# Kernel optimization log

Measured on AMD Instinct MI355X. Metric: run time of the kernel, lower is better.

## Reference

```python
import jax, jax.numpy as jnp
import numpy as np

N, Wt, Tt, DIM = 16, 256, 2048, 256
EPS = 1e-5

def silu(x):
    return x * jax.nn.sigmoid(x)

def setup_inputs() -> dict:
    key = jax.random.key(0)
    ks = jax.random.split(key, 12)
    d = {}
    d['T'] = jnp.arange(Tt, dtype=jnp.float32)
    d['durations'] = jax.random.uniform(ks[0], (N, Wt, 1), jnp.float32)
    d['features'] = jax.random.normal(ks[1], (N, Wt, DIM), jnp.float32)
    d['conv1_w'] = jax.random.normal(ks[2], (8, DIM, 3), jnp.float32) * 0.05
    d['conv1_b'] = jnp.zeros((8,), jnp.float32)
    d['bn1_g'] = jnp.ones((8,), jnp.float32)
    d['bn1_b'] = jnp.zeros((8,), jnp.float32)
    d['bn1_m'] = jnp.zeros((8,), jnp.float32)
    d['bn1_v'] = jnp.ones((8,), jnp.float32)
    d['conv2_w'] = jax.random.normal(ks[3], (8, DIM, 3), jnp.float32) * 0.05
    d['conv2_b'] = jnp.zeros((8,), jnp.float32)
    d['bn2_g'] = jnp.ones((8,), jnp.float32)
    d['bn2_b'] = jnp.zeros((8,), jnp.float32)
    d['bn2_m'] = jnp.zeros((8,), jnp.float32)
    d['bn2_v'] = jnp.ones((8,), jnp.float32)
    d['sb1_w1'] = jax.random.normal(ks[4], (10, 2), jnp.float32) * 0.3
    d['sb1_b1'] = jnp.zeros((2,), jnp.float32)
    d['sb1_w2'] = jax.random.normal(ks[5], (2, 2), jnp.float32) * 0.3
    d['sb1_b2'] = jnp.zeros((2,), jnp.float32)
    d['sb2_w1'] = jax.random.normal(ks[6], (10, 16), jnp.float32) * 0.3
    d['sb2_b1'] = jnp.zeros((16,), jnp.float32)
    d['sb2_w2'] = jax.random.normal(ks[7], (16, 16), jnp.float32) * 0.3
    d['sb2_b2'] = jnp.zeros((16,), jnp.float32)
    d['proj1_w'] = jax.random.normal(ks[8], (2, DIM), jnp.float32) * 0.3
    d['proj1_b'] = jnp.zeros((DIM,), jnp.float32)
    d['proj2_w'] = jax.random.normal(ks[9], (16, 1), jnp.float32) * 0.3
    d['proj2_b'] = jnp.zeros((1,), jnp.float32)
    return d

def _conv_bn_silu(x_ncw, w, b, g, beta, m, v):
    # Conv1d(dim->8, k=3, pad=1) + BatchNorm(eval) + SiLU
    y = jax.lax.conv_general_dilated(x_ncw, w, (1,), [(1, 1)],
                                     dimension_numbers=('NCH', 'OIH', 'NCH'))
    y = y + b[None, :, None]
    y = (y - m[None, :, None]) * jax.lax.rsqrt(v[None, :, None] + EPS)
    y = y * g[None, :, None] + beta[None, :, None]
    return silu(y)

def _swish_block(x, w1, b1, w2, b2):
    x = silu(x @ w1 + b1)
    return silu(x @ w2 + b2)

def reference(T, durations, features, conv1_w, conv1_b, bn1_g, bn1_b, bn1_m, bn1_v,
              conv2_w, conv2_b, bn2_g, bn2_b, bn2_m, bn2_v,
              sb1_w1, sb1_b1, sb1_w2, sb1_b2, sb2_w1, sb2_b1, sb2_w2, sb2_b2,
              proj1_w, proj1_b, proj2_w, proj2_b):
    feat = jnp.swapaxes(features, 1, 2)  # (N, C, W)
    n, _, w = feat.shape
    t = T.shape[0]
    left = jnp.swapaxes(_conv_bn_silu(feat, conv1_w, conv1_b, bn1_g, bn1_b, bn1_m, bn1_v), 1, 2)   # (N, W, 8)
    right = jnp.swapaxes(_conv_bn_silu(feat, conv2_w, conv2_b, bn2_g, bn2_b, bn2_m, bn2_v), 1, 2)  # (N, W, 8)
    token_end = jnp.cumsum(durations, axis=1)        # (N, W, 1)
    token_start = token_end - durations              # (N, W, 1)
    S = T[None, None, :] - token_start               # (N, W, T)
    E = token_end - T[None, None, :]                 # (N, W, T)
    left_b = jnp.broadcast_to(left[:, :, None, :], (n, w, t, 8))
    right_b = jnp.broadcast_to(right[:, :, None, :], (n, w, t, 8))
    xleft = jnp.concatenate([S[..., None], E[..., None], left_b], axis=-1)    # (N, W, T, 10)
    xright = jnp.concatenate([S[..., None], E[..., None], right_b], axis=-1)  # (N, W, T, 10)
    C = _swish_block(xleft, sb1_w1, sb1_b1, sb1_w2, sb1_b2)                   # (N, W, T, 2)
    xr = _swish_block(xright, sb2_w1, sb2_b1, sb2_w2, sb2_b2)                 # (N, W, T, 16)
    score = (xr @ proj2_w + proj2_b)[..., 0]                                  # (N, W, T)
    Wsm = jax.nn.softmax(score, axis=1)  # softmax over tokens W
    out_r = jnp.einsum('nkt,ndk->ntd', Wsm, feat)                             # (N, T, dim)
    out_l = jnp.einsum('nkt,nktp->ntp', Wsm, C) @ proj1_w + proj1_b           # (N, T, dim)
    return out_l + out_r
```

## Files before the change

kernel.cpp:

```cpp
#include <hip/hip_runtime.h>
#include <hip/hip_bf16.h>

#define NN  16
#define WT  256
#define TT  2048
#define DIM 256
#define TBT 8

typedef __attribute__((ext_vector_type(8))) short short8_t;
typedef __attribute__((ext_vector_type(4))) float f32x4;

__device__ __forceinline__ float fast_rcp(float x){ return __builtin_amdgcn_rcpf(x); }

__device__ __forceinline__ float silu_f(float x){
    return x * fast_rcp(1.0f + __expf(-x));
}

__device__ __forceinline__ unsigned short f2bf(float x){
    union { float f; unsigned u; } v; v.f = x;
    unsigned r = v.u + 0x7FFFu + ((v.u >> 16) & 1u);
    return (unsigned short)(r >> 16);
}

__device__ __forceinline__ void fma4(float4& a, float s, const float4& f){
    a.x = fmaf(s, f.x, a.x); a.y = fmaf(s, f.y, a.y);
    a.z = fmaf(s, f.z, a.z); a.w = fmaf(s, f.w, a.w);
}

__global__ __launch_bounds__(WT) void cumsum_k(const float* __restrict__ dur,
                                               float* __restrict__ ts,
                                               float* __restrict__ te){
    int n = blockIdx.x, w = threadIdx.x;
    __shared__ float s[WT];
    float d = dur[n*WT + w];
    s[w] = d;
    __syncthreads();
    for (int off = 1; off < WT; off <<= 1){
        float v = (w >= off) ? s[w-off] : 0.0f;
        __syncthreads();
        s[w] += v;
        __syncthreads();
    }
    float e = s[w];
    te[n*WT + w] = e;
    ts[n*WT + w] = e - d;
}

__global__ __launch_bounds__(256) void prep_k(
    const float* __restrict__ feat,
    const float* __restrict__ c1w, const float* __restrict__ c1b,
    const float* __restrict__ g1,  const float* __restrict__ be1,
    const float* __restrict__ m1,  const float* __restrict__ vv1,
    const float* __restrict__ c2w, const float* __restrict__ c2b,
    const float* __restrict__ g2,  const float* __restrict__ be2,
    const float* __restrict__ m2,  const float* __restrict__ vv2,
    const float* __restrict__ sb1w1, const float* __restrict__ sb1b1,
    const float* __restrict__ sb2w1, const float* __restrict__ sb2b1,
    const float* __restrict__ ts, const float* __restrict__ te,
    float* __restrict__ v1o, float* __restrict__ v2o)
{
    int w = blockIdx.x, n = blockIdx.y;
    int tid = threadIdx.x;
    const float* fb = feat + (size_t)(n*WT)*DIM;
    float fm = (w > 0)    ? fb[(size_t)(w-1)*DIM + tid] : 0.0f;
    float f0 =              fb[(size_t) w   *DIM + tid];
    float fp = (w < WT-1) ? fb[(size_t)(w+1)*DIM + tid] : 0.0f;

    float pl[8], pr[8];
    #pragma unroll
    for (int o = 0; o < 8; o++){
        const float* wp = c1w + (size_t)(o*DIM + tid)*3;
        pl[o] = fmaf(fm, wp[0], fmaf(f0, wp[1], fp*wp[2]));
        const float* wq = c2w + (size_t)(o*DIM + tid)*3;
        pr[o] = fmaf(fm, wq[0], fmaf(f0, wq[1], fp*wq[2]));
    }
    #pragma unroll
    for (int o = 0; o < 8; o++){
        #pragma unroll
        for (int off = 32; off; off >>= 1){
            pl[o] += __shfl_xor(pl[o], off);
            pr[o] += __shfl_xor(pr[o], off);
        }
    }
    __shared__ float sws[4][16];
    int wave = tid >> 6, lane = tid & 63;
    if (lane == 0){
        #pragma unroll
        for (int o = 0; o < 8; o++){ sws[wave][o] = pl[o]; sws[wave][8+o] = pr[o]; }
    }
    __syncthreads();
    __shared__ float slr[16];
    if (tid < 16){
        float s = sws[0][tid] + sws[1][tid] + sws[2][tid] + sws[3][tid];
        int o = tid & 7; bool isr = tid >= 8;
        float bias = isr ? c2b[o] : c1b[o];
        float mm   = isr ? m2[o]  : m1[o];
        float vv   = isr ? vv2[o] : vv1[o];
        float gg   = isr ? g2[o]  : g1[o];
        float bb   = isr ? be2[o] : be1[o];
        float y = s + bias;
        y = (y - mm) * rsqrtf(vv + 1e-5f);
        y = y * gg + bb;
        slr[tid] = silu_f(y);
    }
    __syncthreads();
    float start = ts[n*WT + w], end = te[n*WT + w];
    if (tid < 16){
        int j = tid;
        float acc = sb2b1[j] - start*sb2w1[j] + end*sb2w1[16 + j];
        #pragma unroll
        for (int o = 0; o < 8; o++) acc = fmaf(slr[8+o], sb2w1[(2+o)*16 + j], acc);
        v2o[(size_t)(n*WT + w)*16 + j] = acc;
    } else if (tid < 18){
        int p = tid - 16;
        float acc = sb1b1[p] - start*sb1w1[p] + end*sb1w1[2 + p];
        #pragma unroll
        for (int o = 0; o < 8; o++) acc = fmaf(slr[o], sb1w1[(2+o)*2 + p], acc);
        v1o[(size_t)(n*WT + w)*2 + p] = acc;
    }
}

__global__ __launch_bounds__(256) void featpack_k(const float* __restrict__ feat,
                                                  unsigned short* __restrict__ featP)
{
    int kb = blockIdx.x, n = blockIdx.y;
    int d = threadIdx.x;
    const float* fb = feat + (size_t)n*WT*DIM + (size_t)kb*32*DIM + d;
    unsigned short* op = featP + ((size_t)(n*8 + kb)*DIM + d)*32;
    unsigned short buf[32];
    #pragma unroll
    for (int e = 0; e < 32; e++) buf[e] = f2bf(fb[(size_t)e*DIM]);
    #pragma unroll
    for (int g = 0; g < 4; g++){
        uint4 u;
        u.x = (unsigned)buf[g*8+0] | ((unsigned)buf[g*8+1] << 16);
        u.y = (unsigned)buf[g*8+2] | ((unsigned)buf[g*8+3] << 16);
        u.z = (unsigned)buf[g*8+4] | ((unsigned)buf[g*8+5] << 16);
        u.w = (unsigned)buf[g*8+6] | ((unsigned)buf[g*8+7] << 16);
        *(uint4*)(op + g*8) = u;
    }
}

__global__ __launch_bounds__(256) void score_k(
    const float* __restrict__ Tg,
    const float* __restrict__ v1g, const float* __restrict__ v2g,
    const float* __restrict__ sb1w1, const float* __restrict__ sb1w2, const float* __restrict__ sb1b2,
    const float* __restrict__ sb2w1, const float* __restrict__ sb2w2, const float* __restrict__ sb2b2,
    const float* __restrict__ p2w, const float* __restrict__ p2b,
    unsigned short* __restrict__ wsm_b, float* __restrict__ wc_g)
{
    int n   = blockIdx.y;
    int t0  = blockIdx.x * TBT;
    int tid = threadIdx.x;
    int w   = tid;
    int lane = tid & 63, wave = tid >> 6;

    __shared__ float s_w2[16*16];
    __shared__ float s_u2[16], s_b2[16], s_p2w[16];
    __shared__ float s_u1[2], s_w21[4], s_b21[2];
    __shared__ float s_xa[4][TBT];
    __shared__ float s_xs[4][TBT];
    __shared__ float s_xc0[4][TBT], s_xc1[4][TBT];

    s_w2[tid] = sb2w2[tid];
    if (tid < 16){
        s_u2[tid]  = sb2w1[tid] - sb2w1[16 + tid];
        s_b2[tid]  = sb2b2[tid];
        s_p2w[tid] = p2w[tid];
    } else if (tid < 18){
        int p = tid - 16;
        s_u1[p]  = sb1w1[p] - sb1w1[2 + p];
        s_b21[p] = sb1b2[p];
    } else if (tid < 22){
        s_w21[tid - 18] = sb1w2[tid - 18];
    }
    __syncthreads();

    float v2r[16];
    {
        const float4* vp = (const float4*)(v2g + (size_t)(n*WT + w)*16);
        float4 a = vp[0], b = vp[1], c = vp[2], d = vp[3];
        v2r[0]=a.x; v2r[1]=a.y; v2r[2]=a.z; v2r[3]=a.w;
        v2r[4]=b.x; v2r[5]=b.y; v2r[6]=b.z; v2r[7]=b.w;
        v2r[8]=c.x; v2r[9]=c.y; v2r[10]=c.z; v2r[11]=c.w;
        v2r[12]=d.x; v2r[13]=d.y; v2r[14]=d.z; v2r[15]=d.w;
    }
    float v1r0, v1r1;
    {
        const float* vp = v1g + (size_t)(n*WT + w)*2;
        v1r0 = vp[0]; v1r1 = vp[1];
    }
    float p2bv = p2b[0];
    float tv[TBT];
    #pragma unroll
    for (int ti = 0; ti < TBT; ti++) tv[ti] = Tg[t0 + ti];

    float scores[TBT];
    #pragma unroll
    for (int tp = 0; tp < TBT; tp += 2){
        float h2a[16], h2b[16];
        #pragma unroll
        for (int j = 0; j < 16; j++){ float b = s_b2[j]; h2a[j] = b; h2b[j] = b; }
        #pragma unroll
        for (int i = 0; i < 16; i++){
            float u = s_u2[i], v = v2r[i];
            float aa = silu_f(fmaf(tv[tp],   u, v));
            float ab = silu_f(fmaf(tv[tp+1], u, v));
            #pragma unroll
            for (int j = 0; j < 16; j++){
                float wv = s_w2[i*16 + j];
                h2a[j] = fmaf(aa, wv, h2a[j]);
                h2b[j] = fmaf(ab, wv, h2b[j]);
            }
        }
        float sa = p2bv, sb = p2bv;
        #pragma unroll
        for (int j = 0; j < 16; j++){
            float pw = s_p2w[j];
            sa = fmaf(silu_f(h2a[j]), pw, sa);
            sb = fmaf(silu_f(h2b[j]), pw, sb);
        }
        scores[tp] = sa; scores[tp+1] = sb;
    }

    float c0r[TBT], c1r[TBT];
    {
        float u10 = s_u1[0], u11 = s_u1[1];
        float w00 = s_w21[0], w01 = s_w21[1], w10 = s_w21[2], w11 = s_w21[3];
        float b0 = s_b21[0], b1 = s_b21[1];
        #pragma unroll
        for (int ti = 0; ti < TBT; ti++){
            float gl0 = silu_f(fmaf(tv[ti], u10, v1r0));
            float gl1 = silu_f(fmaf(tv[ti], u11, v1r1));
            c0r[ti] = silu_f(fmaf(gl0, w00, fmaf(gl1, w10, b0)));
            c1r[ti] = silu_f(fmaf(gl0, w01, fmaf(gl1, w11, b1)));
        }
    }

    float m[TBT];
    #pragma unroll
    for (int ti = 0; ti < TBT; ti++) m[ti] = scores[ti];
    #pragma unroll
    for (int off = 32; off; off >>= 1){
        #pragma unroll
        for (int ti = 0; ti < TBT; ti++) m[ti] = fmaxf(m[ti], __shfl_xor(m[ti], off));
    }
    if (lane == 0){
        #pragma unroll
        for (int ti = 0; ti < TBT; ti++) s_xa[wave][ti] = m[ti];
    }
    __syncthreads();
    #pragma unroll
    for (int ti = 0; ti < TBT; ti++)
        m[ti] = fmaxf(fmaxf(s_xa[0][ti], s_xa[1][ti]), fmaxf(s_xa[2][ti], s_xa[3][ti]));

    float e[TBT], ps[TBT], pc0[TBT], pc1[TBT];
    #pragma unroll
    for (int ti = 0; ti < TBT; ti++){
        e[ti]   = __expf(scores[ti] - m[ti]);
        ps[ti]  = e[ti];
        pc0[ti] = e[ti] * c0r[ti];
        pc1[ti] = e[ti] * c1r[ti];
    }
    #pragma unroll
    for (int off = 32; off; off >>= 1){
        #pragma unroll
        for (int ti = 0; ti < TBT; ti++){
            ps[ti]  += __shfl_xor(ps[ti],  off);
            pc0[ti] += __shfl_xor(pc0[ti], off);
            pc1[ti] += __shfl_xor(pc1[ti], off);
        }
    }
    if (lane == 0){
        #pragma unroll
        for (int ti = 0; ti < TBT; ti++){
            s_xs[wave][ti]  = ps[ti];
            s_xc0[wave][ti] = pc0[ti];
            s_xc1[wave][ti] = pc1[ti];
        }
    }
    __syncthreads();

    unsigned short* wbase = wsm_b + ((size_t)n*TT + t0)*WT + w;
    #pragma unroll
    for (int ti = 0; ti < TBT; ti++){
        float S  = s_xs[0][ti] + s_xs[1][ti] + s_xs[2][ti] + s_xs[3][ti];
        float rS = fast_rcp(S);
        wbase[(size_t)ti*WT] = f2bf(e[ti] * rS);
    }
    if (tid < TBT){
        int ti = tid;
        float S  = s_xs[0][ti] + s_xs[1][ti] + s_xs[2][ti] + s_xs[3][ti];
        float rS = fast_rcp(S);
        float2 wc;
        wc.x = (s_xc0[0][ti] + s_xc0[1][ti] + s_xc0[2][ti] + s_xc0[3][ti]) * rS;
        wc.y = (s_xc1[0][ti] + s_xc1[1][ti] + s_xc1[2][ti] + s_xc1[3][ti]) * rS;
        *(float2*)(wc_g + ((size_t)n*TT + t0 + ti)*2) = wc;
    }
}

__global__ __launch_bounds__(256) void outr_mfma_k(
    const unsigned short* __restrict__ wsmB, const unsigned short* __restrict__ featP,
    const float* __restrict__ wc_g,
    const float* __restrict__ p1w, const float* __restrict__ p1b,
    float* __restrict__ out)
{
    int n    = blockIdx.y;
    int t0   = blockIdx.x * 64;
    int tid  = threadIdx.x;
    int lane = tid & 63, wave = tid >> 6;
    int tw   = t0 + wave*16;
    int l15  = lane & 15, quad = lane >> 4;

    f32x4 acc[16];
    #pragma unroll
    for (int dt = 0; dt < 16; dt++) acc[dt] = (f32x4){0.f, 0.f, 0.f, 0.f};

    const unsigned short* aPtr = wsmB + ((size_t)(n*TT + tw + l15))*WT + quad*8;

    #pragma unroll
    for (int kb = 0; kb < 8; kb++){
        short8_t af = *(const short8_t*)(aPtr + kb*32);
        const unsigned short* bp = featP + ((size_t)(n*8 + kb)*DIM + l15)*32 + quad*8;
        #pragma unroll
        for (int dt = 0; dt < 16; dt++){
            short8_t bf = *(const short8_t*)(bp + (size_t)dt*16*32);
            acc[dt] = __builtin_amdgcn_mfma_f32_16x16x32_bf16(af, bf, acc[dt], 0, 0, 0);
        }
    }

    float wc0[4], wc1[4];
    #pragma unroll
    for (int r = 0; r < 4; r++){
        const float* wp = wc_g + ((size_t)(n*TT + tw + quad*4 + r))*2;
        wc0[r] = wp[0]; wc1[r] = wp[1];
    }
    float* obase = out + ((size_t)(n*TT + tw + quad*4))*DIM;
    #pragma unroll
    for (int dt = 0; dt < 16; dt++){
        int d = dt*16 + l15;
        float pa = p1w[d], pb2 = p1w[DIM + d], pc = p1b[d];
        #pragma unroll
        for (int r = 0; r < 4; r++){
            float val = acc[dt][r] + fmaf(wc0[r], pa, fmaf(wc1[r], pb2, pc));
            obase[(size_t)r*DIM + d] = val;
        }
    }
}

__global__ __launch_bounds__(256) void fused_k(
    const float* __restrict__ Tg, const float* __restrict__ feat,
    const float* __restrict__ v1g, const float* __restrict__ v2g,
    const float* __restrict__ sb1w1, const float* __restrict__ sb1w2, const float* __restrict__ sb1b2,
    const float* __restrict__ sb2w1, const float* __restrict__ sb2w2, const float* __restrict__ sb2b2,
    const float* __restrict__ p1w, const float* __restrict__ p1b,
    const float* __restrict__ p2w, const float* __restrict__ p2b,
    float* __restrict__ out)
{
    int n   = blockIdx.y;
    int t0  = blockIdx.x * TBT;
    int tid = threadIdx.x;
    int w   = tid;
    int lane = tid & 63, wave = tid >> 6;

    __shared__ float s_w2[16*16];
    __shared__ float s_u2[16], s_b2[16], s_p2w[16];
    __shared__ float s_u1[2], s_w21[4], s_b21[2];
    __shared__ float s_wsmT[WT][TBT];
    __shared__ float s_xa[4][TBT];
    __shared__ float s_xs[4][TBT];
    __shared__ float s_xc0[4][TBT], s_xc1[4][TBT];
    __shared__ float s_wc0[TBT], s_wc1[TBT];
    __shared__ float s_out[4][DIM];

    s_w2[tid] = sb2w2[tid];
    if (tid < 16){
        s_u2[tid]  = sb2w1[tid] - sb2w1[16 + tid];
        s_b2[tid]  = sb2b2[tid];
        s_p2w[tid] = p2w[tid];
    } else if (tid < 18){
        int p = tid - 16;
        s_u1[p]  = sb1w1[p] - sb1w1[2 + p];
        s_b21[p] = sb1b2[p];
    } else if (tid < 22){
        s_w21[tid - 18] = sb1w2[tid - 18];
    }
    __syncthreads();

    float v2r[16];
    {
        const float4* vp = (const float4*)(v2g + (size_t)(n*WT + w)*16);
        float4 a = vp[0], b = vp[1], c = vp[2], d = vp[3];
        v2r[0]=a.x; v2r[1]=a.y; v2r[2]=a.z; v2r[3]=a.w;
        v2r[4]=b.x; v2r[5]=b.y; v2r[6]=b.z; v2r[7]=b.w;
        v2r[8]=c.x; v2r[9]=c.y; v2r[10]=c.z; v2r[11]=c.w;
        v2r[12]=d.x; v2r[13]=d.y; v2r[14]=d.z; v2r[15]=d.w;
    }
    float v1r0, v1r1;
    {
        const float* vp = v1g + (size_t)(n*WT + w)*2;
        v1r0 = vp[0]; v1r1 = vp[1];
    }
    float p2bv = p2b[0];
    float tv[TBT];
    #pragma unroll
    for (int ti = 0; ti < TBT; ti++) tv[ti] = Tg[t0 + ti];

    float scores[TBT];
    #pragma unroll
    for (int tp = 0; tp < TBT; tp += 2){
        float h2a[16], h2b[16];
        #pragma unroll
        for (int j = 0; j < 16; j++){ float b = s_b2[j]; h2a[j] = b; h2b[j] = b; }
        #pragma unroll
        for (int i = 0; i < 16; i++){
            float u = s_u2[i], v = v2r[i];
            float aa = silu_f(fmaf(tv[tp],   u, v));
            float ab = silu_f(fmaf(tv[tp+1], u, v));
            #pragma unroll
            for (int j = 0; j < 16; j++){
                float wv = s_w2[i*16 + j];
                h2a[j] = fmaf(aa, wv, h2a[j]);
                h2b[j] = fmaf(ab, wv, h2b[j]);
            }
        }
        float sa = p2bv, sb = p2bv;
        #pragma unroll
        for (int j = 0; j < 16; j++){
            float pw = s_p2w[j];
            sa = fmaf(silu_f(h2a[j]), pw, sa);
            sb = fmaf(silu_f(h2b[j]), pw, sb);
        }
        scores[tp] = sa; scores[tp+1] = sb;
    }

    float c0r[TBT], c1r[TBT];
    {
        float u10 = s_u1[0], u11 = s_u1[1];
        float w00 = s_w21[0], w01 = s_w21[1], w10 = s_w21[2], w11 = s_w21[3];
        float b0 = s_b21[0], b1 = s_b21[1];
        #pragma unroll
        for (int ti = 0; ti < TBT; ti++){
            float gl0 = silu_f(fmaf(tv[ti], u10, v1r0));
            float gl1 = silu_f(fmaf(tv[ti], u11, v1r1));
            c0r[ti] = silu_f(fmaf(gl0, w00, fmaf(gl1, w10, b0)));
            c1r[ti] = silu_f(fmaf(gl0, w01, fmaf(gl1, w11, b1)));
        }
    }

    float m[TBT];
    #pragma unroll
    for (int ti = 0; ti < TBT; ti++) m[ti] = scores[ti];
    #pragma unroll
    for (int off = 32; off; off >>= 1){
        #pragma unroll
        for (int ti = 0; ti < TBT; ti++) m[ti] = fmaxf(m[ti], __shfl_xor(m[ti], off));
    }
    if (lane == 0){
        #pragma unroll
        for (int ti = 0; ti < TBT; ti++) s_xa[wave][ti] = m[ti];
    }
    __syncthreads();
    #pragma unroll
    for (int ti = 0; ti < TBT; ti++)
        m[ti] = fmaxf(fmaxf(s_xa[0][ti], s_xa[1][ti]), fmaxf(s_xa[2][ti], s_xa[3][ti]));

    float e[TBT], ps[TBT], pc0[TBT], pc1[TBT];
    #pragma unroll
    for (int ti = 0; ti < TBT; ti++){
        e[ti]  = __expf(scores[ti] - m[ti]);
        ps[ti] = e[ti];
        pc0[ti] = e[ti] * c0r[ti];
        pc1[ti] = e[ti] * c1r[ti];
    }
    #pragma unroll
    for (int off = 32; off; off >>= 1){
        #pragma unroll
        for (int ti = 0; ti < TBT; ti++){
            ps[ti]  += __shfl_xor(ps[ti],  off);
            pc0[ti] += __shfl_xor(pc0[ti], off);
            pc1[ti] += __shfl_xor(pc1[ti], off);
        }
    }
    if (lane == 0){
        #pragma unroll
        for (int ti = 0; ti < TBT; ti++){
            s_xs[wave][ti]  = ps[ti];
            s_xc0[wave][ti] = pc0[ti];
            s_xc1[wave][ti] = pc1[ti];
        }
    }
    __syncthreads();
    #pragma unroll
    for (int ti = 0; ti < TBT; ti++){
        float S  = s_xs[0][ti] + s_xs[1][ti] + s_xs[2][ti] + s_xs[3][ti];
        float rS = fast_rcp(S);
        s_wsmT[w][ti] = e[ti] * rS;
    }
    if (tid < TBT){
        int ti = tid;
        float S  = s_xs[0][ti] + s_xs[1][ti] + s_xs[2][ti] + s_xs[3][ti];
        float rS = fast_rcp(S);
        s_wc0[ti] = (s_xc0[0][ti] + s_xc0[1][ti] + s_xc0[2][ti] + s_xc0[3][ti]) * rS;
        s_wc1[ti] = (s_xc1[0][ti] + s_xc1[1][ti] + s_xc1[2][ti] + s_xc1[3][ti]) * rS;
    }
    __syncthreads();

    int wid = wave;
    int dq  = lane;
    const float* fbase = feat + (size_t)n*WT*DIM + dq*4;
    float4 acc[TBT];
    #pragma unroll
    for (int i = 0; i < TBT; i++) acc[i] = make_float4(0.f, 0.f, 0.f, 0.f);

    #pragma unroll 4
    for (int w0 = wid; w0 < WT; w0 += 4){
        float4 f = *(const float4*)(fbase + (size_t)w0*DIM);
        const float4* wp = (const float4*)&s_wsmT[w0][0];
        float4 wA = wp[0], wB = wp[1];
        fma4(acc[0], wA.x, f); fma4(acc[1], wA.y, f);
        fma4(acc[2], wA.z, f); fma4(acc[3], wA.w, f);
        fma4(acc[4], wB.x, f); fma4(acc[5], wB.y, f);
        fma4(acc[6], wB.z, f); fma4(acc[7], wB.w, f);
    }

    float pw0 = p1w[tid], pw1 = p1w[DIM + tid], pbv = p1b[tid];
    float* orow = out + ((size_t)n*TT + t0)*DIM;
    #pragma unroll
    for (int ti = 0; ti < TBT; ti++){
        __syncthreads();
        *(float4*)&s_out[wid][dq*4] = acc[ti];
        __syncthreads();
        float r = s_out[0][tid] + s_out[1][tid] + s_out[2][tid] + s_out[3][tid];
        float o = fmaf(s_wc0[ti], pw0, fmaf(s_wc1[ti], pw1, r + pbv));
        orow[(size_t)ti*DIM + tid] = o;
    }
}

extern "C" void kernel_launch(void* const* d_in, const int* in_sizes, int n_in,
                              void* d_out, int out_size, void* d_ws, size_t ws_size,
                              hipStream_t stream)
{
    const float* Tg    = (const float*)d_in[0];
    const float* dur   = (const float*)d_in[1];
    const float* feat  = (const float*)d_in[2];
    const float* c1w   = (const float*)d_in[3];
    const float* c1b   = (const float*)d_in[4];
    const float* bn1g  = (const float*)d_in[5];
    const float* bn1b  = (const float*)d_in[6];
    const float* bn1m  = (const float*)d_in[7];
    const float* bn1v  = (const float*)d_in[8];
    const float* c2w   = (const float*)d_in[9];
    const float* c2b   = (const float*)d_in[10];
    const float* bn2g  = (const float*)d_in[11];
    const float* bn2b  = (const float*)d_in[12];
    const float* bn2m  = (const float*)d_in[13];
    const float* bn2v  = (const float*)d_in[14];
    const float* sb1w1 = (const float*)d_in[15];
    const float* sb1b1 = (const float*)d_in[16];
    const float* sb1w2 = (const float*)d_in[17];
    const float* sb1b2 = (const float*)d_in[18];
    const float* sb2w1 = (const float*)d_in[19];
    const float* sb2b1 = (const float*)d_in[20];
    const float* sb2w2 = (const float*)d_in[21];
    const float* sb2b2 = (const float*)d_in[22];
    const float* p1w   = (const float*)d_in[23];
    const float* p1b   = (const float*)d_in[24];
    const float* p2w   = (const float*)d_in[25];
    const float* p2b   = (const float*)d_in[26];
    float* out = (float*)d_out;

    float* ws = (float*)d_ws;
    float* ts  = ws;
    float* te  = ws + 4096;
    float* v1  = ws + 8192;
    float* v2  = ws + 16384;
    float* wc  = ws + 16384 + 65536;
    unsigned short* wsmB  = (unsigned short*)(ws + 16384 + 65536 + 65536);
    unsigned short* featP = wsmB + (size_t)NN*TT*WT;
    size_t need = ((size_t)16384 + 65536 + 65536)*sizeof(float)
                + ((size_t)NN*TT*WT + (size_t)NN*WT*DIM)*sizeof(unsigned short);

    cumsum_k<<<NN, WT, 0, stream>>>(dur, ts, te);
    prep_k<<<dim3(WT, NN), 256, 0, stream>>>(feat, c1w, c1b, bn1g, bn1b, bn1m, bn1v,
                                             c2w, c2b, bn2g, bn2b, bn2m, bn2v,
                                             sb1w1, sb1b1, sb2w1, sb2b1, ts, te, v1, v2);
    if (ws_size >= need){
        featpack_k<<<dim3(8, NN), 256, 0, stream>>>(feat, featP);
        score_k<<<dim3(TT/TBT, NN), 256, 0, stream>>>(Tg, v1, v2,
                                                      sb1w1, sb1w2, sb1b2,
                                                      sb2w1, sb2w2, sb2b2,
                                                      p2w, p2b, wsmB, wc);
        outr_mfma_k<<<dim3(TT/64, NN), 256, 0, stream>>>(wsmB, featP, wc, p1w, p1b, out);
    } else {
        fused_k<<<dim3(TT/TBT, NN), 256, 0, stream>>>(Tg, feat, v1, v2,
                                                      sb1w1, sb1w2, sb1b2,
                                                      sb2w1, sb2w2, sb2b2,
                                                      p1w, p1b, p2w, p2b, out);
    }
}
```

Measured before the change: 310.4 us.

## Fuse score softmax and MFMA output into one kernel via LDS-staged weights

Merges the score/softmax kernel and the MFMA output kernel. Each block now covers 16 time steps and keeps the bf16 softmax weights and the wc terms in shared memory instead of writing them to global memory and reading them back. The block's four waves then each compute a 16x64 slice of the output with MFMA from the LDS tile. This removes the global round trip for the N*T*W weight matrix and one kernel launch. In exchange, each block reads the packed features for its small time tile, which means more repeated feature loads, and register pressure rises from the doubled time tile.

```diff
diff --git a/kernel.cpp b/kernel.cpp
--- a/kernel.cpp
+++ b/kernel.cpp
@@ -6,6 +6,7 @@
 #define TT  2048
 #define DIM 256
 #define TBT 8
+#define TBS 16
 
 typedef __attribute__((ext_vector_type(8))) short short8_t;
 typedef __attribute__((ext_vector_type(4))) float f32x4;
@@ -141,16 +142,18 @@
     }
 }
 
-__global__ __launch_bounds__(256) void score_k(
+__global__ __launch_bounds__(256) void scoreout_k(
     const float* __restrict__ Tg,
     const float* __restrict__ v1g, const float* __restrict__ v2g,
     const float* __restrict__ sb1w1, const float* __restrict__ sb1w2, const float* __restrict__ sb1b2,
     const float* __restrict__ sb2w1, const float* __restrict__ sb2w2, const float* __restrict__ sb2b2,
     const float* __restrict__ p2w, const float* __restrict__ p2b,
-    unsigned short* __restrict__ wsm_b, float* __restrict__ wc_g)
+    const unsigned short* __restrict__ featP,
+    const float* __restrict__ p1w, const float* __restrict__ p1b,
+    float* __restrict__ out)
 {
     int n   = blockIdx.y;
-    int t0  = blockIdx.x * TBT;
+    int t0  = blockIdx.x * TBS;
     int tid = threadIdx.x;
     int w   = tid;
     int lane = tid & 63, wave = tid >> 6;
@@ -158,9 +161,11 @@
     __shared__ float s_w2[16*16];
     __shared__ float s_u2[16], s_b2[16], s_p2w[16];
     __shared__ float s_u1[2], s_w21[4], s_b21[2];
-    __shared__ float s_xa[4][TBT];
-    __shared__ float s_xs[4][TBT];
-    __shared__ float s_xc0[4][TBT], s_xc1[4][TBT];
+    __shared__ float s_xa[4][TBS];
+    __shared__ float s_xs[4][TBS];
+    __shared__ float s_xc0[4][TBS], s_xc1[4][TBS];
+    __shared__ unsigned short s_wsmT[TBS][WT + 8];
+    __shared__ float s_wc0[TBS], s_wc1[TBS];
 
     s_w2[tid] = sb2w2[tid];
     if (tid < 16){
@@ -191,13 +196,13 @@
         v1r0 = vp[0]; v1r1 = vp[1];
     }
     float p2bv = p2b[0];
-    float tv[TBT];
-    #pragma unroll
-    for (int ti = 0; ti < TBT; ti++) tv[ti] = Tg[t0 + ti];
-
-    float scores[TBT];
-    #pragma unroll
-    for (int tp = 0; tp < TBT; tp += 2){
+    float tv[TBS];
+    #pragma unroll
+    for (int ti = 0; ti < TBS; ti++) tv[ti] = Tg[t0 + ti];
+
+    float scores[TBS];
+    #pragma unroll
+    for (int tp = 0; tp < TBS; tp += 2){
         float h2a[16], h2b[16];
         #pragma unroll
         for (int j = 0; j < 16; j++){ float b = s_b2[j]; h2a[j] = b; h2b[j] = b; }
@@ -223,13 +228,13 @@
         scores[tp] = sa; scores[tp+1] = sb;
     }
 
-    float c0r[TBT], c1r[TBT];
+    float c0r[TBS], c1r[TBS];
     {
         float u10 = s_u1[0], u11 = s_u1[1];
         float w00 = s_w21[0], w01 = s_w21[1], w10 = s_w21[2], w11 = s_w21[3];
         float b0 = s_b21[0], b1 = s_b21[1];
         #pragma unroll
-        for (int ti = 0; ti < TBT; ti++){
+        for (int ti = 0; ti < TBS; ti++){
             float gl0 = silu_f(fmaf(tv[ti], u10, v1r0));
             float gl1 = silu_f(fmaf(tv[ti], u11, v1r1));
             c0r[ti] = silu_f(fmaf(gl0, w00, fmaf(gl1, w10, b0)));
@@ -237,93 +242,79 @@
         }
     }
 
-    float m[TBT];
-    #pragma unroll
-    for (int ti = 0; ti < TBT; ti++) m[ti] = scores[ti];
+    float m[TBS];
+    #pragma unroll
+    for (int ti = 0; ti < TBS; ti++) m[ti] = scores[ti];
     #pragma unroll
     for (int off = 32; off; off >>= 1){
         #pragma unroll
-        for (int ti = 0; ti < TBT; ti++) m[ti] = fmaxf(m[ti], __shfl_xor(m[ti], off));
+        for (int ti = 0; ti < TBS; ti++) m[ti] = fmaxf(m[ti], __shfl_xor(m[ti], off));
     }
     if (lane == 0){
         #pragma unroll
-        for (int ti = 0; ti < TBT; ti++) s_xa[wave][ti] = m[ti];
-    }
-    __syncthreads();
-    #pragma unroll
-    for (int ti = 0; ti < TBT; ti++)
+        for (int ti = 0; ti < TBS; ti++) s_xa[wave][ti] = m[ti];
+    }
+    __syncthreads();
+    #pragma unroll
+    for (int ti = 0; ti < TBS; ti++)
         m[ti] = fmaxf(fmaxf(s_xa[0][ti], s_xa[1][ti]), fmaxf(s_xa[2][ti], s_xa[3][ti]));
 
-    float e[TBT], ps[TBT], pc0[TBT], pc1[TBT];
-    #pragma unroll
-    for (int ti = 0; ti < TBT; ti++){
-        e[ti]   = __expf(scores[ti] - m[ti]);
-        ps[ti]  = e[ti];
-        pc0[ti] = e[ti] * c0r[ti];
-        pc1[ti] = e[ti] * c1r[ti];
+    #pragma unroll
+    for (int ti = 0; ti < TBS; ti++){
+        float e = __expf(scores[ti] - m[ti]);
+        scores[ti] = e;
+        m[ti]   = e;
+        c0r[ti] = e * c0r[ti];
+        c1r[ti] = e * c1r[ti];
     }
     #pragma unroll
     for (int off = 32; off; off >>= 1){
         #pragma unroll
-        for (int ti = 0; ti < TBT; ti++){
-            ps[ti]  += __shfl_xor(ps[ti],  off);
-            pc0[ti] += __shfl_xor(pc0[ti], off);
-            pc1[ti] += __shfl_xor(pc1[ti], off);
+        for (int ti = 0; ti < TBS; ti++){
+            m[ti]   += __shfl_xor(m[ti],   off);
+            c0r[ti] += __shfl_xor(c0r[ti], off);
+            c1r[ti] += __shfl_xor(c1r[ti], off);
         }
     }
     if (lane == 0){
         #pragma unroll
-        for (int ti = 0; ti < TBT; ti++){
-            s_xs[wave][ti]  = ps[ti];
-            s_xc0[wave][ti] = pc0[ti];
-            s_xc1[wave][ti] = pc1[ti];
-        }
-    }
-    __syncthreads();
-
-    unsigned short* wbase = wsm_b + ((size_t)n*TT + t0)*WT + w;
-    #pragma unroll
-    for (int ti = 0; ti < TBT; ti++){
+        for (int ti = 0; ti < TBS; ti++){
+            s_xs[wave][ti]  = m[ti];
+            s_xc0[wave][ti] = c0r[ti];
+            s_xc1[wave][ti] = c1r[ti];
+        }
+    }
+    __syncthreads();
+
+    #pragma unroll
+    for (int ti = 0; ti < TBS; ti++){
         float S  = s_xs[0][ti] + s_xs[1][ti] + s_xs[2][ti] + s_xs[3][ti];
         float rS = fast_rcp(S);
-        wbase[(size_t)ti*WT] = f2bf(e[ti] * rS);
-    }
-    if (tid < TBT){
+        s_wsmT[ti][w] = f2bf(scores[ti] * rS);
+    }
+    if (tid < TBS){
         int ti = tid;
         float S  = s_xs[0][ti] + s_xs[1][ti] + s_xs[2][ti] + s_xs[3][ti];
         float rS = fast_rcp(S);
-        float2 wc;
-        wc.x = (s_xc0[0][ti] + s_xc0[1][ti] + s_xc0[2][ti] + s_xc0[3][ti]) * rS;
-        wc.y = (s_xc1[0][ti] + s_xc1[1][ti] + s_xc1[2][ti] + s_xc1[3][ti]) * rS;
-        *(float2*)(wc_g + ((size_t)n*TT + t0 + ti)*2) = wc;
-    }
-}
-
-__global__ __launch_bounds__(256) void outr_mfma_k(
-    const unsigned short* __restrict__ wsmB, const unsigned short* __restrict__ featP,
-    const float* __restrict__ wc_g,
-    const float* __restrict__ p1w, const float* __restrict__ p1b,
-    float* __restrict__ out)
-{
-    int n    = blockIdx.y;
-    int t0   = blockIdx.x * 64;
-    int tid  = threadIdx.x;
-    int lane = tid & 63, wave = tid >> 6;
-    int tw   = t0 + wave*16;
-    int l15  = lane & 15, quad = lane >> 4;
-
-    f32x4 acc[16];
-    #pragma unroll
-    for (int dt = 0; dt < 16; dt++) acc[dt] = (f32x4){0.f, 0.f, 0.f, 0.f};
-
-    const unsigned short* aPtr = wsmB + ((size_t)(n*TT + tw + l15))*WT + quad*8;
-
+        s_wc0[ti] = (s_xc0[0][ti] + s_xc0[1][ti] + s_xc0[2][ti] + s_xc0[3][ti]) * rS;
+        s_wc1[ti] = (s_xc1[0][ti] + s_xc1[1][ti] + s_xc1[2][ti] + s_xc1[3][ti]) * rS;
+    }
+    __syncthreads();
+
+    int l15 = lane & 15, quad = lane >> 4;
+    int dbase = wave * 4;
+
+    f32x4 acc[4];
+    #pragma unroll
+    for (int dt = 0; dt < 4; dt++) acc[dt] = (f32x4){0.f, 0.f, 0.f, 0.f};
+
+    const unsigned short* aRow = &s_wsmT[l15][0];
     #pragma unroll
     for (int kb = 0; kb < 8; kb++){
-        short8_t af = *(const short8_t*)(aPtr + kb*32);
-        const unsigned short* bp = featP + ((size_t)(n*8 + kb)*DIM + l15)*32 + quad*8;
-        #pragma unroll
-        for (int dt = 0; dt < 16; dt++){
+        short8_t af = *(const short8_t*)(aRow + kb*32 + quad*8);
+        const unsigned short* bp = featP + ((size_t)(n*8 + kb)*DIM + dbase*16 + l15)*32 + quad*8;
+        #pragma unroll
+        for (int dt = 0; dt < 4; dt++){
             short8_t bf = *(const short8_t*)(bp + (size_t)dt*16*32);
             acc[dt] = __builtin_amdgcn_mfma_f32_16x16x32_bf16(af, bf, acc[dt], 0, 0, 0);
         }
@@ -332,13 +323,13 @@
     float wc0[4], wc1[4];
     #pragma unroll
     for (int r = 0; r < 4; r++){
-        const float* wp = wc_g + ((size_t)(n*TT + tw + quad*4 + r))*2;
-        wc0[r] = wp[0]; wc1[r] = wp[1];
-    }
-    float* obase = out + ((size_t)(n*TT + tw + quad*4))*DIM;
-    #pragma unroll
-    for (int dt = 0; dt < 16; dt++){
-        int d = dt*16 + l15;
+        wc0[r] = s_wc0[quad*4 + r];
+        wc1[r] = s_wc1[quad*4 + r];
+    }
+    float* obase = out + ((size_t)(n*TT + t0 + quad*4))*DIM;
+    #pragma unroll
+    for (int dt = 0; dt < 4; dt++){
+        int d = (dbase + dt)*16 + l15;
         float pa = p1w[d], pb2 = p1w[DIM + d], pc = p1b[d];
         #pragma unroll
         for (int r = 0; r < 4; r++){
@@ -575,11 +566,9 @@
     float* te  = ws + 4096;
     float* v1  = ws + 8192;
     float* v2  = ws + 16384;
-    float* wc  = ws + 16384 + 65536;
-    unsigned short* wsmB  = (unsigned short*)(ws + 16384 + 65536 + 65536);
-    unsigned short* featP = wsmB + (size_t)NN*TT*WT;
-    size_t need = ((size_t)16384 + 65536 + 65536)*sizeof(float)
-                + ((size_t)NN*TT*WT + (size_t)NN*WT*DIM)*sizeof(unsigned short);
+    unsigned short* featP = (unsigned short*)(ws + 16384 + 65536);
+    size_t need = ((size_t)16384 + 65536)*sizeof(float)
+                + (size_t)NN*WT*DIM*sizeof(unsigned short);
 
     cumsum_k<<<NN, WT, 0, stream>>>(dur, ts, te);
     prep_k<<<dim3(WT, NN), 256, 0, stream>>>(feat, c1w, c1b, bn1g, bn1b, bn1m, bn1v,
@@ -587,11 +576,10 @@
                                              sb1w1, sb1b1, sb2w1, sb2b1, ts, te, v1, v2);
     if (ws_size >= need){
         featpack_k<<<dim3(8, NN), 256, 0, stream>>>(feat, featP);
-        score_k<<<dim3(TT/TBT, NN), 256, 0, stream>>>(Tg, v1, v2,
-                                                      sb1w1, sb1w2, sb1b2,
-                                                      sb2w1, sb2w2, sb2b2,
-                                                      p2w, p2b, wsmB, wc);
-        outr_mfma_k<<<dim3(TT/64, NN), 256, 0, stream>>>(wsmB, featP, wc, p1w, p1b, out);
+        scoreout_k<<<dim3(TT/TBS, NN), 256, 0, stream>>>(Tg, v1, v2,
+                                                         sb1w1, sb1w2, sb1b2,
+                                                         sb2w1, sb2w2, sb2b2,
+                                                         p2w, p2b, featP, p1w, p1b, out);
     } else {
         fused_k<<<dim3(TT/TBT, NN), 256, 0, stream>>>(Tg, feat, v1, v2,
                                                       sb1w1, sb1w2, sb1b2,
```

After: 376.1 us. 1.21x slower.
